# Optimization experiments

Measured on AMD Instinct MI355X. Metric: run time of the kernel, lower is better.

## Reference

```python
import jax, jax.numpy as jnp
import numpy as np

N, K, N_OF, N_EF, H = 16384, 32, 7, 1, 1


def setup_inputs() -> dict:
    key = jax.random.key(0)
    ks = jax.random.split(key, 8)
    return {
        "object_features": jax.random.normal(ks[0], (N, K, N_OF), dtype=jnp.float32),
        "edge_features": jax.random.uniform(ks[1], (N, K, K, N_EF), dtype=jnp.float32),
        "action": jax.random.normal(ks[2], (N, N_OF), dtype=jnp.float32),
        "W_ni": jax.random.normal(ks[3], (2 * N_OF, H), dtype=jnp.float32) / np.sqrt(2 * N_OF),
        "b_ni": jnp.zeros((H,), dtype=jnp.float32),
        "W_e": jax.random.normal(ks[4], (2 * H + N_EF, H), dtype=jnp.float32) / np.sqrt(2 * H + N_EF),
        "b_e": jnp.zeros((H,), dtype=jnp.float32),
        "W_n": jax.random.normal(ks[5], (H, H), dtype=jnp.float32),
        "b_n": jnp.zeros((H,), dtype=jnp.float32),
        "W_ef": jax.random.normal(ks[6], (H, N_EF), dtype=jnp.float32),
        "b_ef": jnp.zeros((N_EF,), dtype=jnp.float32),
    }


def reference(object_features, edge_features, action, W_ni, b_ni, W_e, b_e, W_n, b_n, W_ef, b_ef):
    n, k, _ = object_features.shape
    # embed: concat node features with broadcast action, Linear (no activation)
    a = jnp.broadcast_to(action[:, None, :], object_features.shape)  # (N,K,n_of)
    xa = jnp.concatenate([object_features, a], axis=-1)              # (N,K,2*n_of)
    hn = xa @ W_ni + b_ni                                            # (N,K,H)

    def edge_fn(hn):
        x = jnp.broadcast_to(hn[:, :, None, :], (n, k, k, hn.shape[-1]))  # sender
        xxe = jnp.concatenate([x, jnp.swapaxes(x, 1, 2), edge_features], axis=-1)
        return jax.nn.relu(xxe @ W_e + b_e)                          # (N,K,K,H)

    # one message-passing round (I = 1)
    he = edge_fn(hn)
    hn = jax.nn.relu(he.sum(axis=2) @ W_n + b_n)                     # (N,K,H)
    # final edge update + edge readout
    he = edge_fn(hn)
    hef = jax.nn.relu(he @ W_ef + b_ef)                              # (N,K,K,n_ef)
    return jax.nn.sigmoid(hef)  # pred_type == 'full_state'
```

## Files before the change

### kernel.cpp

```cpp
#include <hip/hip_runtime.h>
#include <math.h>


typedef float v4f __attribute__((ext_vector_type(4)));

#define DPP_ADD(p, ctrl)                                                  \
    ((p) + __int_as_float(__builtin_amdgcn_mov_dpp(                       \
               __float_as_int(p), (ctrl), 0xf, 0xf, true)))

__global__ __launch_bounds__(256) void gnn_fused_kernel(
    const float* __restrict__ of,
    const float* __restrict__ ef,
    const float* __restrict__ act,
    const float* __restrict__ W_ni,
    const float* __restrict__ b_ni,
    const float* __restrict__ W_e,
    const float* __restrict__ b_e,
    const float* __restrict__ W_n,
    const float* __restrict__ b_n,
    const float* __restrict__ W_ef,
    const float* __restrict__ b_ef,
    float* __restrict__ out,
    int Ntot)
{
    const int wv = threadIdx.x >> 6;
    const int l  = threadIdx.x & 63;
    const int n  = blockIdx.x * 4 + wv;
    if (n >= Ntot) return;

    __shared__ __align__(16) float sh_hn[4][32];
    __shared__ __align__(16) float sh_hn2[4][32];
    float* hn_lds  = sh_hn[wv];
    float* hn2_lds = sh_hn2[wv];

    const float* efp = ef + (size_t)n * 1024 + l * 4;
    const float4 e0 = *reinterpret_cast<const float4*>(efp);
    const float4 e1 = *reinterpret_cast<const float4*>(efp + 256);
    const float4 e2 = *reinterpret_cast<const float4*>(efp + 512);
    const float4 e3 = *reinterpret_cast<const float4*>(efp + 768);

    const float we0 = W_e[0], we1 = W_e[1], we2 = W_e[2], be = b_e[0];
    const float wn  = W_n[0],  bn  = b_n[0];
    const float wef = W_ef[0], bef = b_ef[0];

    {
        const float* ofp = of + ((size_t)n * 32 + (l & 31)) * 7;
        const float* ap  = act + (size_t)n * 7;
        float s = b_ni[0];
        #pragma unroll
        for (int f = 0; f < 7; ++f) s = fmaf(ofp[f], W_ni[f], s);
        #pragma unroll
        for (int f = 0; f < 7; ++f) s = fmaf(ap[f], W_ni[7 + f], s);
        hn_lds[l & 31] = s;
    }
    __builtin_amdgcn_wave_barrier();

    const int m     = l >> 3;
    const int jbase = (l & 7) * 4;

    const float4 hj = *reinterpret_cast<const float4*>(&hn_lds[jbase]);
    const float hi0 = hn_lds[m];
    const float hi1 = hn_lds[m + 8];
    const float hi2 = hn_lds[m + 16];
    const float hi3 = hn_lds[m + 24];

    auto rowsum = [&](const float4& e, float hi) {
        const float a = fmaf(we0, hi, be);
        float p = fmaxf(fmaf(we2, e.x, fmaf(we1, hj.x, a)), 0.f)
                + fmaxf(fmaf(we2, e.y, fmaf(we1, hj.y, a)), 0.f)
                + fmaxf(fmaf(we2, e.z, fmaf(we1, hj.z, a)), 0.f)
                + fmaxf(fmaf(we2, e.w, fmaf(we1, hj.w, a)), 0.f);
        p = DPP_ADD(p, 0xB1);
        p = DPP_ADD(p, 0x4E);
        p = DPP_ADD(p, 0x141);
        return p;
    };
    const float s0 = rowsum(e0, hi0);
    const float s1 = rowsum(e1, hi1);
    const float s2 = rowsum(e2, hi2);
    const float s3 = rowsum(e3, hi3);

    const float g0 = fmaxf(fmaf(wn, s0, bn), 0.f);
    const float g1 = fmaxf(fmaf(wn, s1, bn), 0.f);
    const float g2 = fmaxf(fmaf(wn, s2, bn), 0.f);
    const float g3 = fmaxf(fmaf(wn, s3, bn), 0.f);

    if ((l & 7) == 0) {
        hn2_lds[m]      = g0;
        hn2_lds[m + 8]  = g1;
        hn2_lds[m + 16] = g2;
        hn2_lds[m + 24] = g3;
    }
    __builtin_amdgcn_wave_barrier();
    const float4 gj = *reinterpret_cast<const float4*>(&hn2_lds[jbase]);

    float* outp = out + (size_t)n * 1024 + l * 4;
    auto edge2 = [&](const float4& e, float gi, float* dst) {
        const float a = fmaf(we0, gi, be);
        v4f o;
        {
            float v = fmaxf(fmaf(we2, e.x, fmaf(we1, gj.x, a)), 0.f);
            v = fmaxf(fmaf(wef, v, bef), 0.f);
            o.x = __builtin_amdgcn_rcpf(1.f + __builtin_amdgcn_exp2f(v * -1.44269504089f));
        }
        {
            float v = fmaxf(fmaf(we2, e.y, fmaf(we1, gj.y, a)), 0.f);
            v = fmaxf(fmaf(wef, v, bef), 0.f);
            o.y = __builtin_amdgcn_rcpf(1.f + __builtin_amdgcn_exp2f(v * -1.44269504089f));
        }
        {
            float v = fmaxf(fmaf(we2, e.z, fmaf(we1, gj.z, a)), 0.f);
            v = fmaxf(fmaf(wef, v, bef), 0.f);
            o.z = __builtin_amdgcn_rcpf(1.f + __builtin_amdgcn_exp2f(v * -1.44269504089f));
        }
        {
            float v = fmaxf(fmaf(we2, e.w, fmaf(we1, gj.w, a)), 0.f);
            v = fmaxf(fmaf(wef, v, bef), 0.f);
            o.w = __builtin_amdgcn_rcpf(1.f + __builtin_amdgcn_exp2f(v * -1.44269504089f));
        }
        __builtin_nontemporal_store(o, (v4f*)dst);
    };
    edge2(e0, g0, outp);
    edge2(e1, g1, outp + 256);
    edge2(e2, g2, outp + 512);
    edge2(e3, g3, outp + 768);
}

extern "C" void kernel_launch(void* const* d_in, const int* in_sizes, int n_in,
                              void* d_out, int out_size, void* d_ws, size_t ws_size,
                              hipStream_t stream) {
    const float* of   = (const float*)d_in[0];
    const float* ef   = (const float*)d_in[1];
    const float* act  = (const float*)d_in[2];
    const float* W_ni = (const float*)d_in[3];
    const float* b_ni = (const float*)d_in[4];
    const float* W_e  = (const float*)d_in[5];
    const float* b_e  = (const float*)d_in[6];
    const float* W_n  = (const float*)d_in[7];
    const float* b_n  = (const float*)d_in[8];
    const float* W_ef = (const float*)d_in[9];
    const float* b_ef = (const float*)d_in[10];
    float* out = (float*)d_out;

    const int N = in_sizes[2] / 7;
    const int blocks = (N + 3) / 4;
    gnn_fused_kernel<<<blocks, 256, 0, stream>>>(
        of, ef, act, W_ni, b_ni, W_e, b_e, W_n, b_n, W_ef, b_ef, out, N);
}
```

Baseline: 27.39 us.

## Process two graphs per wave, prefetching the second graph's edges into LDS

Each wave now handles two graphs (n and n+N/2). While the first graph's output is computed and stored, the second graph's edge features are loaded straight into LDS with global_load_lds, and its node features go into registers. The aim is to hide load latency behind compute and stores and to halve the number of blocks. In exchange it adds 16KB of LDS per block, a hand-written vmcnt wait that relies on the order of memory operations, and a launch_bounds occupancy hint.

```diff
diff --git a/kernel.cpp b/kernel.cpp
--- a/kernel.cpp
+++ b/kernel.cpp
@@ -8,7 +8,14 @@
     ((p) + __int_as_float(__builtin_amdgcn_mov_dpp(                       \
                __float_as_int(p), (ctrl), 0xf, 0xf, true)))
 
-__global__ __launch_bounds__(256) void gnn_fused_kernel(
+__device__ __forceinline__ void glds16(const float* gsrc, float* ldst) {
+    __builtin_amdgcn_global_load_lds(
+        (const __attribute__((address_space(1))) void*)gsrc,
+        (__attribute__((address_space(3))) void*)ldst,
+        16, 0, 0);
+}
+
+__global__ __launch_bounds__(256, 6) void gnn_fused_kernel(
     const float* __restrict__ of,
     const float* __restrict__ ef,
     const float* __restrict__ act,
@@ -21,109 +28,159 @@
     const float* __restrict__ W_ef,
     const float* __restrict__ b_ef,
     float* __restrict__ out,
-    int Ntot)
+    int Ntot, int halfN)
 {
     const int wv = threadIdx.x >> 6;
     const int l  = threadIdx.x & 63;
-    const int n  = blockIdx.x * 4 + wv;
-    if (n >= Ntot) return;
+    const int nA = blockIdx.x * 4 + wv;
+    if (nA >= halfN) return;
+    const int nB = nA + halfN;
+    const bool hasB = (nB < Ntot);
 
     __shared__ __align__(16) float sh_hn[4][32];
     __shared__ __align__(16) float sh_hn2[4][32];
+    __shared__ __align__(16) float sh_ef[4][1024];
     float* hn_lds  = sh_hn[wv];
     float* hn2_lds = sh_hn2[wv];
-
-    const float* efp = ef + (size_t)n * 1024 + l * 4;
-    const float4 e0 = *reinterpret_cast<const float4*>(efp);
-    const float4 e1 = *reinterpret_cast<const float4*>(efp + 256);
-    const float4 e2 = *reinterpret_cast<const float4*>(efp + 512);
-    const float4 e3 = *reinterpret_cast<const float4*>(efp + 768);
+    float* efst    = sh_ef[wv];
+
+    const int m     = l >> 3;
+    const int jbase = (l & 7) * 4;
 
     const float we0 = W_e[0], we1 = W_e[1], we2 = W_e[2], be = b_e[0];
     const float wn  = W_n[0],  bn  = b_n[0];
     const float wef = W_ef[0], bef = b_ef[0];
-
+    const float bni = b_ni[0];
+
+    const float* efpA = ef + (size_t)nA * 1024 + l * 4;
+    const float4 a0 = *reinterpret_cast<const float4*>(efpA);
+    const float4 a1 = *reinterpret_cast<const float4*>(efpA + 256);
+    const float4 a2 = *reinterpret_cast<const float4*>(efpA + 512);
+    const float4 a3 = *reinterpret_cast<const float4*>(efpA + 768);
+
+    float hnA;
     {
-        const float* ofp = of + ((size_t)n * 32 + (l & 31)) * 7;
-        const float* ap  = act + (size_t)n * 7;
-        float s = b_ni[0];
+        const float* ofp = of + ((size_t)nA * 32 + (l & 31)) * 7;
+        const float* ap  = act + (size_t)nA * 7;
+        float s = bni;
         #pragma unroll
         for (int f = 0; f < 7; ++f) s = fmaf(ofp[f], W_ni[f], s);
         #pragma unroll
         for (int f = 0; f < 7; ++f) s = fmaf(ap[f], W_ni[7 + f], s);
-        hn_lds[l & 31] = s;
+        hnA = s;
     }
-    __builtin_amdgcn_wave_barrier();
-
-    const int m     = l >> 3;
-    const int jbase = (l & 7) * 4;
-
-    const float4 hj = *reinterpret_cast<const float4*>(&hn_lds[jbase]);
-    const float hi0 = hn_lds[m];
-    const float hi1 = hn_lds[m + 8];
-    const float hi2 = hn_lds[m + 16];
-    const float hi3 = hn_lds[m + 24];
-
-    auto rowsum = [&](const float4& e, float hi) {
-        const float a = fmaf(we0, hi, be);
-        float p = fmaxf(fmaf(we2, e.x, fmaf(we1, hj.x, a)), 0.f)
-                + fmaxf(fmaf(we2, e.y, fmaf(we1, hj.y, a)), 0.f)
-                + fmaxf(fmaf(we2, e.z, fmaf(we1, hj.z, a)), 0.f)
-                + fmaxf(fmaf(we2, e.w, fmaf(we1, hj.w, a)), 0.f);
-        p = DPP_ADD(p, 0xB1);
-        p = DPP_ADD(p, 0x4E);
-        p = DPP_ADD(p, 0x141);
-        return p;
+
+    auto pass1 = [&](const float4& e0, const float4& e1, const float4& e2,
+                     const float4& e3, float hn_own,
+                     float& g0, float& g1, float& g2, float& g3, float4& gj) {
+        hn_lds[l & 31] = hn_own;
+        __builtin_amdgcn_wave_barrier();
+        const float4 hj = *reinterpret_cast<const float4*>(&hn_lds[jbase]);
+        const float hi0 = hn_lds[m];
+        const float hi1 = hn_lds[m + 8];
+        const float hi2 = hn_lds[m + 16];
+        const float hi3 = hn_lds[m + 24];
+
+        auto rowsum = [&](const float4& e, float hi) {
+            const float a = fmaf(we0, hi, be);
+            float p = fmaxf(fmaf(we2, e.x, fmaf(we1, hj.x, a)), 0.f)
+                    + fmaxf(fmaf(we2, e.y, fmaf(we1, hj.y, a)), 0.f)
+                    + fmaxf(fmaf(we2, e.z, fmaf(we1, hj.z, a)), 0.f)
+                    + fmaxf(fmaf(we2, e.w, fmaf(we1, hj.w, a)), 0.f);
+            p = DPP_ADD(p, 0xB1);
+            p = DPP_ADD(p, 0x4E);
+            p = DPP_ADD(p, 0x141);
+            return p;
+        };
+        g0 = fmaxf(fmaf(wn, rowsum(e0, hi0), bn), 0.f);
+        g1 = fmaxf(fmaf(wn, rowsum(e1, hi1), bn), 0.f);
+        g2 = fmaxf(fmaf(wn, rowsum(e2, hi2), bn), 0.f);
+        g3 = fmaxf(fmaf(wn, rowsum(e3, hi3), bn), 0.f);
+
+        if ((l & 7) == 0) {
+            hn2_lds[m]      = g0;
+            hn2_lds[m + 8]  = g1;
+            hn2_lds[m + 16] = g2;
+            hn2_lds[m + 24] = g3;
+        }
+        __builtin_amdgcn_wave_barrier();
+        gj = *reinterpret_cast<const float4*>(&hn2_lds[jbase]);
     };
-    const float s0 = rowsum(e0, hi0);
-    const float s1 = rowsum(e1, hi1);
-    const float s2 = rowsum(e2, hi2);
-    const float s3 = rowsum(e3, hi3);
-
-    const float g0 = fmaxf(fmaf(wn, s0, bn), 0.f);
-    const float g1 = fmaxf(fmaf(wn, s1, bn), 0.f);
-    const float g2 = fmaxf(fmaf(wn, s2, bn), 0.f);
-    const float g3 = fmaxf(fmaf(wn, s3, bn), 0.f);
-
-    if ((l & 7) == 0) {
-        hn2_lds[m]      = g0;
-        hn2_lds[m + 8]  = g1;
-        hn2_lds[m + 16] = g2;
-        hn2_lds[m + 24] = g3;
+
+    auto pass2 = [&](const float4& e0, const float4& e1, const float4& e2,
+                     const float4& e3, float g0, float g1, float g2, float g3,
+                     const float4& gj, float* outp) {
+        auto edge2 = [&](const float4& e, float gi, float* dst) {
+            const float a = fmaf(we0, gi, be);
+            v4f o;
+            {
+                float v = fmaxf(fmaf(we2, e.x, fmaf(we1, gj.x, a)), 0.f);
+                v = fmaxf(fmaf(wef, v, bef), 0.f);
+                o.x = __builtin_amdgcn_rcpf(1.f + __builtin_amdgcn_exp2f(v * -1.44269504089f));
+            }
+            {
+                float v = fmaxf(fmaf(we2, e.y, fmaf(we1, gj.y, a)), 0.f);
+                v = fmaxf(fmaf(wef, v, bef), 0.f);
+                o.y = __builtin_amdgcn_rcpf(1.f + __builtin_amdgcn_exp2f(v * -1.44269504089f));
+            }
+            {
+                float v = fmaxf(fmaf(we2, e.z, fmaf(we1, gj.z, a)), 0.f);
+                v = fmaxf(fmaf(wef, v, bef), 0.f);
+                o.z = __builtin_amdgcn_rcpf(1.f + __builtin_amdgcn_exp2f(v * -1.44269504089f));
+            }
+            {
+                float v = fmaxf(fmaf(we2, e.w, fmaf(we1, gj.w, a)), 0.f);
+                v = fmaxf(fmaf(wef, v, bef), 0.f);
+                o.w = __builtin_amdgcn_rcpf(1.f + __builtin_amdgcn_exp2f(v * -1.44269504089f));
+            }
+            __builtin_nontemporal_store(o, (v4f*)dst);
+        };
+        edge2(e0, g0, outp);
+        edge2(e1, g1, outp + 256);
+        edge2(e2, g2, outp + 512);
+        edge2(e3, g3, outp + 768);
+    };
+
+    float g0, g1, g2, g3;
+    float4 gjA;
+    pass1(a0, a1, a2, a3, hnA, g0, g1, g2, g3, gjA);
+
+    float ofb[7], actb[7];
+    if (hasB) {
+        const float* efpB = ef + (size_t)nB * 1024 + l * 4;
+        glds16(efpB,       &efst[0]);
+        glds16(efpB + 256, &efst[256]);
+        glds16(efpB + 512, &efst[512]);
+        glds16(efpB + 768, &efst[768]);
+        __builtin_amdgcn_sched_barrier(0);
+        const float* ofpB = of + ((size_t)nB * 32 + (l & 31)) * 7;
+        const float* apB  = act + (size_t)nB * 7;
+        #pragma unroll
+        for (int f = 0; f < 7; ++f) ofb[f] = ofpB[f];
+        #pragma unroll
+        for (int f = 0; f < 7; ++f) actb[f] = apB[f];
+        __builtin_amdgcn_sched_barrier(0);
     }
-    __builtin_amdgcn_wave_barrier();
-    const float4 gj = *reinterpret_cast<const float4*>(&hn2_lds[jbase]);
-
-    float* outp = out + (size_t)n * 1024 + l * 4;
-    auto edge2 = [&](const float4& e, float gi, float* dst) {
-        const float a = fmaf(we0, gi, be);
-        v4f o;
-        {
-            float v = fmaxf(fmaf(we2, e.x, fmaf(we1, gj.x, a)), 0.f);
-            v = fmaxf(fmaf(wef, v, bef), 0.f);
-            o.x = __builtin_amdgcn_rcpf(1.f + __builtin_amdgcn_exp2f(v * -1.44269504089f));
-        }
-        {
-            float v = fmaxf(fmaf(we2, e.y, fmaf(we1, gj.y, a)), 0.f);
-            v = fmaxf(fmaf(wef, v, bef), 0.f);
-            o.y = __builtin_amdgcn_rcpf(1.f + __builtin_amdgcn_exp2f(v * -1.44269504089f));
-        }
-        {
-            float v = fmaxf(fmaf(we2, e.z, fmaf(we1, gj.z, a)), 0.f);
-            v = fmaxf(fmaf(wef, v, bef), 0.f);
-            o.z = __builtin_amdgcn_rcpf(1.f + __builtin_amdgcn_exp2f(v * -1.44269504089f));
-        }
-        {
-            float v = fmaxf(fmaf(we2, e.w, fmaf(we1, gj.w, a)), 0.f);
-            v = fmaxf(fmaf(wef, v, bef), 0.f);
-            o.w = __builtin_amdgcn_rcpf(1.f + __builtin_amdgcn_exp2f(v * -1.44269504089f));
-        }
-        __builtin_nontemporal_store(o, (v4f*)dst);
-    };
-    edge2(e0, g0, outp);
-    edge2(e1, g1, outp + 256);
-    edge2(e2, g2, outp + 512);
-    edge2(e3, g3, outp + 768);
+
+    pass2(a0, a1, a2, a3, g0, g1, g2, g3, gjA, out + (size_t)nA * 1024 + l * 4);
+
+    if (hasB) {
+        float hnB = bni;
+        #pragma unroll
+        for (int f = 0; f < 7; ++f) hnB = fmaf(ofb[f], W_ni[f], hnB);
+        #pragma unroll
+        for (int f = 0; f < 7; ++f) hnB = fmaf(actb[f], W_ni[7 + f], hnB);
+
+        asm volatile("s_waitcnt vmcnt(4)" ::: "memory");
+        const float4 b0 = *reinterpret_cast<const float4*>(&efst[l * 4]);
+        const float4 b1 = *reinterpret_cast<const float4*>(&efst[256 + l * 4]);
+        const float4 b2 = *reinterpret_cast<const float4*>(&efst[512 + l * 4]);
+        const float4 b3 = *reinterpret_cast<const float4*>(&efst[768 + l * 4]);
+
+        float4 gjB;
+        pass1(b0, b1, b2, b3, hnB, g0, g1, g2, g3, gjB);
+        pass2(b0, b1, b2, b3, g0, g1, g2, g3, gjB, out + (size_t)nB * 1024 + l * 4);
+    }
 }
 
 extern "C" void kernel_launch(void* const* d_in, const int* in_sizes, int n_in,
@@ -134,8 +191,8 @@
     const float* act  = (const float*)d_in[2];
     const float* W_ni = (const float*)d_in[3];
     const float* b_ni = (const float*)d_in[4];
+    const float* b_e_ = (const float*)d_in[6];
     const float* W_e  = (const float*)d_in[5];
-    const float* b_e  = (const float*)d_in[6];
     const float* W_n  = (const float*)d_in[7];
     const float* b_n  = (const float*)d_in[8];
     const float* W_ef = (const float*)d_in[9];
@@ -143,7 +200,8 @@
     float* out = (float*)d_out;
 
     const int N = in_sizes[2] / 7;
-    const int blocks = (N + 3) / 4;
+    const int halfN = (N + 1) / 2;
+    const int blocks = (halfN + 3) / 4;
     gnn_fused_kernel<<<blocks, 256, 0, stream>>>(
-        of, ef, act, W_ni, b_ni, W_e, b_e, W_n, b_n, W_ef, b_ef, out, N);
+        of, ef, act, W_ni, b_ni, W_e, b_e_, W_n, b_n, W_ef, b_ef, out, N, halfN);
 }
```

New measurement: 27.63 us. No clear change (+0.9%).
